# Kernel tuning notes

Hardware: AMD Instinct MI355X
Metric: run time of the kernel (lower is better)

The kernel has to match this reference:

```python
import jax, jax.numpy as jnp
import numpy as np

NEG_SLOPE = 0.2  # PyG GATConv default negative_slope
NUM_GRAPHS = 64
N, E, F_IN = 50000, 800000, 128


def _gat(x, src, dst, W, a_s, a_d, b, concat):
    # PyG GATConv: h = x W (per head); e_ij = leaky_relu(a_s.h_j + a_d.h_i);
    # softmax over incoming edges of each dst node; out_i = sum_j alpha_ij h_j
    n = x.shape[0]
    H, C = a_s.shape
    h = (x @ W).reshape(n, H, C)                     # [N,H,C]
    es = jnp.einsum('nhc,hc->nh', h, a_s)            # [N,H]
    ed = jnp.einsum('nhc,hc->nh', h, a_d)
    e = jax.nn.leaky_relu(es[src] + ed[dst], NEG_SLOPE)   # [E,H]
    m = jax.ops.segment_max(e, dst, num_segments=n)       # per-dst max (stable softmax)
    ex = jnp.exp(e - m[dst])
    den = jax.ops.segment_sum(ex, dst, num_segments=n)
    alpha = ex / den[dst]                                 # [E,H]
    out = jax.ops.segment_sum(h[src] * alpha[:, :, None], dst, num_segments=n)  # [N,H,C]
    if concat:
        return out.reshape(n, H * C) + b
    return out.mean(axis=1) + b


def setup_inputs() -> dict:
    key = jax.random.key(0)
    ks = jax.random.split(key, 10)
    x = jax.random.normal(ks[0], (N, F_IN), jnp.float32)
    edge_index = jax.random.randint(ks[1], (2, E), 0, N, dtype=jnp.int64)
    batch = jnp.sort(jax.random.randint(ks[2], (N,), 0, NUM_GRAPHS, dtype=jnp.int64))
    s1 = 1.0 / np.sqrt(F_IN)
    s2 = 1.0 / np.sqrt(256)
    return {
        'x': x,
        'edge_index': edge_index,
        'batch': batch,
        'W1': jax.random.normal(ks[3], (F_IN, 256), jnp.float32) * s1,
        'a_src1': jax.random.normal(ks[4], (4, 64), jnp.float32) * s2,
        'a_dst1': jax.random.normal(ks[5], (4, 64), jnp.float32) * s2,
        'b1': jnp.zeros((256,), jnp.float32),
        'W2': jax.random.normal(ks[6], (256, 128), jnp.float32) * s2,
        'a_src2': jax.random.normal(ks[7], (1, 128), jnp.float32) * (1.0 / np.sqrt(128)),
        'a_dst2': jax.random.normal(ks[8], (1, 128), jnp.float32) * (1.0 / np.sqrt(128)),
        'b2': jnp.zeros((128,), jnp.float32),
        'fc_w': jax.random.normal(ks[9], (128, 10), jnp.float32) * (1.0 / np.sqrt(128)),
        'fc_b': jnp.zeros((10,), jnp.float32),
    }


def reference(x, edge_index, batch, W1, a_src1, a_dst1, b1, W2, a_src2, a_dst2, b2, fc_w, fc_b):
    n = x.shape[0]
    loop = jnp.arange(n, dtype=edge_index.dtype)  # PyG add_self_loops=True
    src = jnp.concatenate([edge_index[0], loop])
    dst = jnp.concatenate([edge_index[1], loop])
    h = jax.nn.elu(_gat(x, src, dst, W1, a_src1, a_dst1, b1, True))   # dropout: eval mode -> identity
    h = jax.nn.elu(_gat(h, src, dst, W2, a_src2, a_dst2, b2, False))
    pooled = jax.ops.segment_sum(h, batch, num_segments=NUM_GRAPHS)
    cnt = jax.ops.segment_sum(jnp.ones((n,), h.dtype), batch, num_segments=NUM_GRAPHS)
    pooled = pooled / jnp.maximum(cnt, 1.0)[:, None]
    logits = pooled @ fc_w + fc_b
    return jax.nn.log_softmax(logits, axis=1)
```

## Files before the change

kernel.cpp:

```cpp
#include <hip/hip_runtime.h>
#include <math.h>

#define N_NODES 50000
#define N_PAD   50048
#define N_EDGES 800000
#define E_TOT   (N_EDGES + N_NODES)
#define NG 64
#define CAP 48
#define NBKT 512
#define BNODES 98
#define RCAP 24
#define FILL_CHUNK 2048
#define GEMM1_BLOCKS 782
#define FILL_BLOCKS  391
#define PH1_TOTAL (GEMM1_BLOCKS + FILL_BLOCKS)
#define G2_NB 16

typedef short short8 __attribute__((ext_vector_type(8)));
typedef float floatx4 __attribute__((ext_vector_type(4)));
typedef float floatx2 __attribute__((ext_vector_type(2)));

__device__ inline short f2bf(float f) {
    union { float f; unsigned u; } v; v.f = f;
    unsigned r = v.u + 0x7fff + ((v.u >> 16) & 1);
    return (short)(r >> 16);
}

__device__ inline unsigned f2fp8(float f) {
    union { float f; unsigned u; } v; v.f = f;
    unsigned s = v.u & 0x80000000u;
    unsigned au = v.u & 0x7fffffffu;
    if (au > 0x43E00000u) au = 0x43E00000u;
    unsigned r = au + 0x7ffffu + ((au >> 20) & 1);
    int e8 = (int)(r >> 23) - 120;
    unsigned m3 = (r >> 20) & 7;
    unsigned code;
    if (e8 <= 0) code = 0;
    else if (e8 > 15) code = 0x7e;
    else code = ((unsigned)e8 << 3) | m3;
    return (s >> 24) | code;
}

__device__ inline float leaky_exp(float t) {
    t = t > 0.f ? t : 0.2f * t;
    return __expf(t);
}

__device__ inline unsigned rfl(unsigned v) {
    return (unsigned)__builtin_amdgcn_readfirstlane((int)v);
}


__global__ __launch_bounds__(256) void phase1_kernel(const float* __restrict__ x,
                                                     const float* __restrict__ W1,
                                                     const float* __restrict__ a_s,
                                                     const float* __restrict__ a_d,
                                                     const int* __restrict__ ei,
                                                     unsigned short* __restrict__ gcnt,
                                                     unsigned* __restrict__ gb2,
                                                     unsigned char* __restrict__ C8,
                                                     float* __restrict__ es,
                                                     float* __restrict__ ed,
                                                     const float* __restrict__ W2,
                                                     const float* __restrict__ as2,
                                                     const float* __restrict__ ad2,
                                                     float* __restrict__ ws2,
                                                     float* __restrict__ wd2,
                                                     float* __restrict__ pooled) {
    __shared__ short bs[64][136];
    __shared__ int hist[NBKT];
    int bid = blockIdx.x;
    int tid = threadIdx.x;

    if (bid == PH1_TOTAL) {
        int k = tid;
        float s = 0.f, d = 0.f;
        for (int c = 0; c < 128; c++) {
            float w = W2[k * 128 + c];
            s += w * as2[c];
            d += w * ad2[c];
        }
        ws2[k] = s;
        wd2[k] = d;
        for (int i = tid; i < NG * 128; i += 256) pooled[i] = 0.f;
        return;
    }

    int gb = -1, fb = -1;
    {
        int g3 = bid / 3, r3 = bid - g3 * 3;
        if (r3 == 2) fb = g3;
        else         gb = g3 * 2 + r3;
    }

    if (fb >= 0) {
        hist[tid] = 0; hist[tid + 256] = 0;
        __syncthreads();
        unsigned meta[8], pay[8];
        int e0 = fb * FILL_CHUNK;
#pragma unroll
        for (int j = 0; j < 8; j++) {
            int t = e0 + j * 256 + tid;
            if (t < N_EDGES) {
                int s = ei[t];
                int d = ei[N_EDGES + t];
                unsigned bkt = (unsigned)d / 98u;
                int dlow = d - (int)bkt * 98;
                int pos = atomicAdd(&hist[bkt], 1);
                meta[j] = (bkt << 16) | (unsigned)pos;
                pay[j] = ((unsigned)s << 9) | (unsigned)dlow;
            } else {
                meta[j] = 0xffffffffu;
            }
        }
        __syncthreads();
        {
            int c0h = hist[tid];        if (c0h > RCAP) c0h = RCAP;
            int c1h = hist[tid + 256];  if (c1h > RCAP) c1h = RCAP;
            gcnt[fb * NBKT + tid] = (unsigned short)c0h;
            gcnt[fb * NBKT + tid + 256] = (unsigned short)c1h;
        }
#pragma unroll
        for (int j = 0; j < 8; j++) {
            if (meta[j] != 0xffffffffu) {
                unsigned bkt = meta[j] >> 16;
                unsigned pos = meta[j] & 0xffffu;
                if (pos < RCAP)
                    gb2[((size_t)bkt * FILL_BLOCKS + fb) * RCAP + pos] = pay[j];
            }
        }
        return;
    }

    const int K = 128, N = 256;
    int tc = tid & 63;
    int tk0s = (tid >> 6) * 32;
    int wid = tid >> 6;
    int lane = tid & 63;
    int m0 = gb * 64 + wid * 16;
    int mr = lane & 15;
    int quad = lane >> 4;
    int kq = quad << 3;
    int arow = m0 + mr; if (arow > N_NODES - 1) arow = N_NODES - 1;
    const float* aptr = x + (size_t)arow * K + kq;
    short8 a[4];
#pragma unroll
    for (int kk = 0; kk < 4; kk++) {
        float4 f0 = *(const float4*)(aptr + kk * 32);
        float4 f1 = *(const float4*)(aptr + kk * 32 + 4);
        a[kk][0] = f2bf(f0.x); a[kk][1] = f2bf(f0.y); a[kk][2] = f2bf(f0.z); a[kk][3] = f2bf(f0.w);
        a[kk][4] = f2bf(f1.x); a[kk][5] = f2bf(f1.y); a[kk][6] = f2bf(f1.z); a[kk][7] = f2bf(f1.w);
    }
    int orow = m0 + (quad << 2);
    for (int head = 0; head < 4; head++) {
        int c0 = head * 64;
        if (head) __syncthreads();
        for (int k = tk0s; k < tk0s + 32; k++)
            bs[tc][k] = f2bf(W1[k * 256 + c0 + tc]);
        __syncthreads();
        floatx4 acc[4] = {{0.f,0.f,0.f,0.f},{0.f,0.f,0.f,0.f},{0.f,0.f,0.f,0.f},{0.f,0.f,0.f,0.f}};
#pragma unroll
        for (int kk = 0; kk < 4; kk++) {
#pragma unroll
            for (int t = 0; t < 4; t++) {
                short8 b = *(const short8*)&bs[t * 16 + mr][kq + kk * 32];
                acc[t] = __builtin_amdgcn_mfma_f32_16x16x32_bf16(a[kk], b, acc[t], 0, 0, 0);
            }
        }
        float asv[4], adv[4];
#pragma unroll
        for (int t = 0; t < 4; t++) {
            asv[t] = a_s[c0 + t * 16 + mr];
            adv[t] = a_d[c0 + t * 16 + mr];
        }
#pragma unroll
        for (int r = 0; r < 4; r++) {
            float ps = acc[0][r] * asv[0] + acc[1][r] * asv[1] + acc[2][r] * asv[2] + acc[3][r] * asv[3];
            float pd = acc[0][r] * adv[0] + acc[1][r] * adv[1] + acc[2][r] * adv[2] + acc[3][r] * adv[3];
#pragma unroll
            for (int off = 8; off >= 1; off >>= 1) {
                ps += __shfl_xor(ps, off);
                pd += __shfl_xor(pd, off);
            }
            if (mr == 0) {
                es[(orow + r) * 4 + head] = ps;
                ed[(orow + r) * 4 + head] = pd;
            }
        }
#pragma unroll
        for (int t = 0; t < 4; t++) {
            int ocol = c0 + t * 16 + mr;
#pragma unroll
            for (int r = 0; r < 4; r++) {
                C8[(size_t)(orow + r) * N + ocol] = (unsigned char)f2fp8(acc[t][r]);
            }
        }
    }
}


__global__ __launch_bounds__(512) void binfill_kernel(const unsigned* __restrict__ gb2,
                                                      const unsigned short* __restrict__ gcnt,
                                                      unsigned short* __restrict__ col,
                                                      int* __restrict__ degT) {
    __shared__ unsigned colL[BNODES * CAP / 2];
    __shared__ int cnt[BNODES];
    __shared__ unsigned short cl[FILL_BLOCKS + 1];
    int b = blockIdx.x, tid = threadIdx.x;
    int nbase = b * BNODES;

    for (int i = tid; i < BNODES * CAP / 8; i += 512) ((uint4*)colL)[i] = make_uint4(0, 0, 0, 0);
    if (tid < FILL_BLOCKS) cl[tid] = gcnt[tid * NBKT + b];
    if (tid < BNODES) cnt[tid] = (nbase + tid < N_NODES) ? 1 : 0;
    __syncthreads();

    if (tid < BNODES) {
        int nn = nbase + tid;
        if (nn < N_NODES) ((unsigned short*)colL)[tid * CAP] = (unsigned short)nn;
    }
    const uint4* src4 = (const uint4*)(gb2 + (size_t)b * FILL_BLOCKS * RCAP);
    for (int r = tid; r < FILL_BLOCKS * RCAP / 4; r += 512) {
        int blk = r / 6;
        int q = r - blk * 6;
        int c = cl[blk];
        if (q * 4 < c) {
            uint4 v = src4[r];
            unsigned vv[4] = {v.x, v.y, v.z, v.w};
#pragma unroll
            for (int j = 0; j < 4; j++) {
                if (q * 4 + j < c) {
                    unsigned p = vv[j];
                    int dlow = (int)(p & 511u);
                    int s = (int)(p >> 9);
                    int sp = atomicAdd(&cnt[dlow], 1);
                    if (sp < CAP) ((unsigned short*)colL)[dlow * CAP + sp] = (unsigned short)s;
                }
            }
        }
    }
    __syncthreads();

    uint4* cb = (uint4*)(col + (size_t)b * BNODES * CAP);
    for (int i = tid; i < BNODES * CAP / 8; i += 512) cb[i] = ((uint4*)colL)[i];
    if (tid < BNODES) {
        int nn = nbase + tid;
        if (nn < N_NODES) degT[nn] = cnt[tid];
    }
}


__global__ __launch_bounds__(256) void gather1_kernel(const unsigned char* __restrict__ h8,
                                                      const int* __restrict__ degT,
                                                      const unsigned short* __restrict__ col,
                                                      const float* __restrict__ es,
                                                      const float* __restrict__ ed,
                                                      const float* __restrict__ bias,
                                                      const float* __restrict__ ws2,
                                                      const float* __restrict__ wd2,
                                                      short* __restrict__ out,
                                                      float* __restrict__ es2,
                                                      float* __restrict__ ed2) {
    __shared__ float wlds[4][CAP * 4];
    int tid = threadIdx.x;
    int wid = tid >> 6;
    int n = __builtin_amdgcn_readfirstlane(blockIdx.x * 4 + wid);
    int l = tid & 63;
    int hh = l >> 4;
    int cnt = degT[n]; cnt = cnt < CAP ? cnt : CAP;
    int cnt8 = (cnt + 7) & ~7;

    const uint4* cp4 = (const uint4*)(col + n * CAP);
    uint4 cw0 = cp4[0], cw1 = cp4[1], cw2 = cp4[2], cw3 = cp4[3], cw4 = cp4[4], cw5 = cp4[5];

    unsigned hvA[8], hvB[8];

#define G1_ISSUE(cw, hv) { \
    unsigned d0 = rfl(cw.x), d1 = rfl(cw.y), d2 = rfl(cw.z), d3 = rfl(cw.w); \
    unsigned i0 = d0 & 0xffffu, i1 = d0 >> 16, i2 = d1 & 0xffffu, i3 = d1 >> 16; \
    unsigned i4 = d2 & 0xffffu, i5 = d2 >> 16, i6 = d3 & 0xffffu, i7 = d3 >> 16; \
    hv[0] = *(const unsigned*)&h8[(size_t)i0 * 256 + l * 4]; \
    hv[1] = *(const unsigned*)&h8[(size_t)i1 * 256 + l * 4]; \
    hv[2] = *(const unsigned*)&h8[(size_t)i2 * 256 + l * 4]; \
    hv[3] = *(const unsigned*)&h8[(size_t)i3 * 256 + l * 4]; \
    hv[4] = *(const unsigned*)&h8[(size_t)i4 * 256 + l * 4]; \
    hv[5] = *(const unsigned*)&h8[(size_t)i5 * 256 + l * 4]; \
    hv[6] = *(const unsigned*)&h8[(size_t)i6 * 256 + l * 4]; \
    hv[7] = *(const unsigned*)&h8[(size_t)i7 * 256 + l * 4]; }

#define G1_CONS(eb, hv) { \
    _Pragma("unroll") \
    for (int j = 0; j < 8; j++) { \
        float w = wlds[wid][((eb) + j) * 4 + hh]; \
        floatx2 lo = __builtin_amdgcn_cvt_pk_f32_fp8(hv[j], false); \
        floatx2 hi = __builtin_amdgcn_cvt_pk_f32_fp8(hv[j], true); \
        den += w; ax += w * lo[0]; ay += w * lo[1]; az += w * hi[0]; aw += w * hi[1]; } }

    G1_ISSUE(cw0, hvA);
    if (cnt8 > 8) G1_ISSUE(cw1, hvB);

    {
        float4 edv = *(const float4*)&ed[n * 4];
        if (l < CAP) {
            int s = col[n * CAP + l];
            float4 ev = *(const float4*)&es[s * 4];
            float4 wv4;
            if (l < cnt) {
                wv4.x = leaky_exp(ev.x + edv.x);
                wv4.y = leaky_exp(ev.y + edv.y);
                wv4.z = leaky_exp(ev.z + edv.z);
                wv4.w = leaky_exp(ev.w + edv.w);
            } else {
                wv4.x = wv4.y = wv4.z = wv4.w = 0.f;
            }
            *(float4*)&wlds[wid][l * 4] = wv4;
        }
    }

    float ax = 0.f, ay = 0.f, az = 0.f, aw = 0.f, den = 0.f;
    G1_CONS(0, hvA);
    if (cnt8 > 8) {
        if (cnt8 > 16) G1_ISSUE(cw2, hvA);
        G1_CONS(8, hvB);
        if (cnt8 > 16) {
            if (cnt8 > 24) G1_ISSUE(cw3, hvB);
            G1_CONS(16, hvA);
            if (cnt8 > 24) {
                if (cnt8 > 32) G1_ISSUE(cw4, hvA);
                G1_CONS(24, hvB);
                if (cnt8 > 32) {
                    if (cnt8 > 40) G1_ISSUE(cw5, hvB);
                    G1_CONS(32, hvA);
                    if (cnt8 > 40) G1_CONS(40, hvB);
                }
            }
        }
    }
#undef G1_ISSUE
#undef G1_CONS

    float inv = 1.0f / den;
    float4 bb = *(const float4*)&bias[l * 4];
    float o0 = ax * inv + bb.x;
    float o1 = ay * inv + bb.y;
    float o2 = az * inv + bb.z;
    float o3 = aw * inv + bb.w;
    o0 = o0 > 0.f ? o0 : __expf(o0) - 1.f;
    o1 = o1 > 0.f ? o1 : __expf(o1) - 1.f;
    o2 = o2 > 0.f ? o2 : __expf(o2) - 1.f;
    o3 = o3 > 0.f ? o3 : __expf(o3) - 1.f;
    short4 ob;
    ob.x = f2bf(o0); ob.y = f2bf(o1); ob.z = f2bf(o2); ob.w = f2bf(o3);
    *(short4*)&out[(size_t)n * 256 + l * 4] = ob;

    float4 s4 = *(const float4*)&ws2[l * 4];
    float4 d4 = *(const float4*)&wd2[l * 4];
    float ps = o0 * s4.x + o1 * s4.y + o2 * s4.z + o3 * s4.w;
    float pd = o0 * d4.x + o1 * d4.y + o2 * d4.z + o3 * d4.w;
#pragma unroll
    for (int off = 32; off >= 1; off >>= 1) {
        ps += __shfl_xor(ps, off);
        pd += __shfl_xor(pd, off);
    }
    if (l == 0) {
        es2[n] = ps;
        ed2[n] = pd;
    }
}


__global__ __launch_bounds__(256) void gemm2_kernel(const short* __restrict__ A,
                                                    const float* __restrict__ W2,
                                                    unsigned char* __restrict__ C8) {
    __shared__ short bs[64][264];
    const int K = 256, N = 128;
    int tid = threadIdx.x;
    int tc = tid & 63;
    int tk0s = (tid >> 6) * 64;
    int wid = tid >> 6;
    int lane = tid & 63;
    int m0 = blockIdx.x * 64 + wid * 16;
    int mr = lane & 15;
    int quad = lane >> 4;
    int kq = quad << 3;
    const short* arow = A + (size_t)(m0 + mr) * K + kq;
    short8 a[8];
#pragma unroll
    for (int kk = 0; kk < 8; kk++) a[kk] = *(const short8*)(arow + kk * 32);
    int orow = m0 + (quad << 2);
    for (int by = 0; by < 2; by++) {
        int c0 = by * 64;
        if (by) __syncthreads();
        for (int k = tk0s; k < tk0s + 64; k++)
            bs[tc][k] = f2bf(W2[k * 128 + c0 + tc]);
        __syncthreads();
        floatx4 acc[4] = {{0.f,0.f,0.f,0.f},{0.f,0.f,0.f,0.f},{0.f,0.f,0.f,0.f},{0.f,0.f,0.f,0.f}};
#pragma unroll
        for (int kk = 0; kk < 8; kk++) {
#pragma unroll
            for (int t = 0; t < 4; t++) {
                short8 b = *(const short8*)&bs[t * 16 + mr][kq + kk * 32];
                acc[t] = __builtin_amdgcn_mfma_f32_16x16x32_bf16(a[kk], b, acc[t], 0, 0, 0);
            }
        }
#pragma unroll
        for (int t = 0; t < 4; t++) {
            int ocol = c0 + t * 16 + mr;
#pragma unroll
            for (int r = 0; r < 4; r++) {
                C8[(size_t)(orow + r) * N + ocol] = (unsigned char)f2fp8(acc[t][r]);
            }
        }
    }
}


__global__ __launch_bounds__(256) void gather2_kernel(const unsigned char* __restrict__ h8,
                                                      const int* __restrict__ deg,
                                                      const unsigned short* __restrict__ col,
                                                      const float* __restrict__ es2,
                                                      const float* __restrict__ ed2,
                                                      const float* __restrict__ bias,
                                                      const int* __restrict__ batch,
                                                      float* __restrict__ pooled) {
    __shared__ float wlds[4][CAP];
    __shared__ float plds[8][128];
    __shared__ int pg[8];
    __shared__ int pcnt;
    int tid = threadIdx.x;
    int wid = tid >> 6;
    int l = tid & 63;
    if (tid == 0) pcnt = 0;
    __syncthreads();

    int c0 = l * 2;
    float2 bb = *(const float2*)&bias[c0];
    int nbase = blockIdx.x * G2_NB + wid * (G2_NB / 4);
    int curg = -1;
    float a0 = 0.f, a1 = 0.f;

    auto flush = [&]() {
        if (curg >= 0) {
            int idx = 0;
            if (l == 0) idx = atomicAdd(&pcnt, 1);
            idx = __shfl(idx, 0);
            if (idx < 8) {
                if (l == 0) pg[idx] = curg;
                plds[idx][c0] = a0;
                plds[idx][c0 + 1] = a1;
            } else {
                atomicAdd(&pooled[curg * 128 + c0], a0);
                atomicAdd(&pooled[curg * 128 + c0 + 1], a1);
            }
        }
    };

    unsigned hvA[8], hvB[8];

#define G2_ISSUE(cw, hv) { \
    unsigned d0 = rfl(cw.x), d1 = rfl(cw.y), d2 = rfl(cw.z), d3 = rfl(cw.w); \
    unsigned i0 = d0 & 0xffffu, i1 = d0 >> 16, i2 = d1 & 0xffffu, i3 = d1 >> 16; \
    unsigned i4 = d2 & 0xffffu, i5 = d2 >> 16, i6 = d3 & 0xffffu, i7 = d3 >> 16; \
    hv[0] = *(const unsigned short*)&h8[(size_t)i0 * 128 + l * 2]; \
    hv[1] = *(const unsigned short*)&h8[(size_t)i1 * 128 + l * 2]; \
    hv[2] = *(const unsigned short*)&h8[(size_t)i2 * 128 + l * 2]; \
    hv[3] = *(const unsigned short*)&h8[(size_t)i3 * 128 + l * 2]; \
    hv[4] = *(const unsigned short*)&h8[(size_t)i4 * 128 + l * 2]; \
    hv[5] = *(const unsigned short*)&h8[(size_t)i5 * 128 + l * 2]; \
    hv[6] = *(const unsigned short*)&h8[(size_t)i6 * 128 + l * 2]; \
    hv[7] = *(const unsigned short*)&h8[(size_t)i7 * 128 + l * 2]; }

#define G2_CONS(eb, hv) { \
    _Pragma("unroll") \
    for (int j = 0; j < 8; j++) { \
        float w = wlds[wid][(eb) + j]; \
        floatx2 lo = __builtin_amdgcn_cvt_pk_f32_fp8(hv[j], false); \
        den += w; ax += w * lo[0]; ay += w * lo[1]; } }

    for (int i = 0; i < G2_NB / 4; i++) {
        int n = nbase + i;
        if (n < N_NODES) {
            int bg = batch[n];
            if (bg != curg) {
                flush();
                curg = bg; a0 = 0.f; a1 = 0.f;
            }
            int cnt = deg[n]; cnt = cnt < CAP ? cnt : CAP;
            int cnt8 = (cnt + 7) & ~7;
            const uint4* cp4 = (const uint4*)(col + n * CAP);
            uint4 cw0 = cp4[0], cw1 = cp4[1], cw2 = cp4[2];
            uint4 cw3 = cp4[3], cw4 = cp4[4], cw5 = cp4[5];
            float ax = 0.f, ay = 0.f, den = 0.f;

            G2_ISSUE(cw0, hvA);
            if (cnt8 > 8) G2_ISSUE(cw1, hvB);

            {
                float edv = ed2[n];
                if (l < CAP) {
                    int s = col[n * CAP + l];
                    float w = (l < cnt) ? leaky_exp(es2[s] + edv) : 0.f;
                    wlds[wid][l] = w;
                }
            }

            G2_CONS(0, hvA);
            if (cnt8 > 8) {
                if (cnt8 > 16) G2_ISSUE(cw2, hvA);
                G2_CONS(8, hvB);
                if (cnt8 > 16) {
                    if (cnt8 > 24) G2_ISSUE(cw3, hvB);
                    G2_CONS(16, hvA);
                    if (cnt8 > 24) {
                        if (cnt8 > 32) G2_ISSUE(cw4, hvA);
                        G2_CONS(24, hvB);
                        if (cnt8 > 32) {
                            if (cnt8 > 40) G2_ISSUE(cw5, hvB);
                            G2_CONS(32, hvA);
                            if (cnt8 > 40) G2_CONS(40, hvB);
                        }
                    }
                }
            }

            float inv = 1.0f / den;
            float o0 = ax * inv + bb.x;
            float o1 = ay * inv + bb.y;
            o0 = o0 > 0.f ? o0 : __expf(o0) - 1.f;
            o1 = o1 > 0.f ? o1 : __expf(o1) - 1.f;
            a0 += o0; a1 += o1;
        }
    }
#undef G2_ISSUE
#undef G2_CONS
    flush();
    __syncthreads();

    int m = pcnt; if (m > 8) m = 8;
    if (tid < 128) {
        for (int e = 0; e < m; e++) {
            int ge = pg[e];
            bool first = true;
            for (int e2 = 0; e2 < e; e2++) if (pg[e2] == ge) first = false;
            if (first) {
                float s = plds[e][tid];
                for (int e3 = e + 1; e3 < m; e3++) if (pg[e3] == ge) s += plds[e3][tid];
                atomicAdd(&pooled[ge * 128 + tid], s);
            }
        }
    }
}


__global__ void fc_kernel(const float* __restrict__ pooled, const int* __restrict__ batch,
                          const float* __restrict__ fcw, const float* __restrict__ fcb,
                          float* __restrict__ out) {
    int g = threadIdx.x;
    if (g >= NG) return;
    int lo = 0, hi = N_NODES;
    while (lo < hi) {
        int mid = (lo + hi) >> 1;
        if (batch[mid] < g) lo = mid + 1; else hi = mid;
    }
    int start = lo;
    lo = start; hi = N_NODES;
    while (lo < hi) {
        int mid = (lo + hi) >> 1;
        if (batch[mid] <= g) lo = mid + 1; else hi = mid;
    }
    int cnt = lo - start;
    float inv = 1.0f / (float)(cnt > 0 ? cnt : 1);

    float lg[10];
#pragma unroll
    for (int j = 0; j < 10; j++) lg[j] = fcb[j];
    for (int k = 0; k < 128; k++) {
        float p = pooled[g * 128 + k] * inv;
#pragma unroll
        for (int j = 0; j < 10; j++) lg[j] += p * fcw[k * 10 + j];
    }
    float m = lg[0];
#pragma unroll
    for (int j = 1; j < 10; j++) m = fmaxf(m, lg[j]);
    float se = 0.f;
#pragma unroll
    for (int j = 0; j < 10; j++) se += __expf(lg[j] - m);
    float lse = m + __logf(se);
#pragma unroll
    for (int j = 0; j < 10; j++) out[g * 10 + j] = lg[j] - lse;
}


extern "C" void kernel_launch(void* const* d_in, const int* in_sizes, int n_in,
                              void* d_out, int out_size, void* d_ws, size_t ws_size,
                              hipStream_t stream) {
    const float* x     = (const float*)d_in[0];
    const int*   ei    = (const int*)d_in[1];
    const int*   batch = (const int*)d_in[2];
    const float* W1    = (const float*)d_in[3];
    const float* as1   = (const float*)d_in[4];
    const float* ad1   = (const float*)d_in[5];
    const float* b1    = (const float*)d_in[6];
    const float* W2    = (const float*)d_in[7];
    const float* as2   = (const float*)d_in[8];
    const float* ad2   = (const float*)d_in[9];
    const float* b2    = (const float*)d_in[10];
    const float* fcw   = (const float*)d_in[11];
    const float* fcb   = (const float*)d_in[12];
    float* out = (float*)d_out;

    char* ws = (char*)d_ws;
    size_t off = 0;
    auto alloc = [&](size_t bytes) -> void* {
        void* p = ws + off;
        off = (off + bytes + 255) & ~(size_t)255;
        return p;
    };
    float* pooled        = (float*)alloc(NG * 128 * 4);
    int* degT            = (int*)alloc((size_t)N_PAD * 4);
    unsigned short* col  = (unsigned short*)alloc((size_t)NBKT * BNODES * CAP * 2);
    unsigned* gb2        = (unsigned*)alloc((size_t)NBKT * FILL_BLOCKS * RCAP * 4);
    unsigned short* gcnt = (unsigned short*)alloc((size_t)FILL_BLOCKS * NBKT * 2);
    float* es1           = (float*)alloc((size_t)N_PAD * 4 * 4);
    float* ed1           = (float*)alloc((size_t)N_PAD * 4 * 4);
    float* es2           = (float*)alloc((size_t)N_PAD * 4);
    float* ed2           = (float*)alloc((size_t)N_PAD * 4);
    float* ws2           = (float*)alloc(256 * 4);
    float* wd2           = (float*)alloc(256 * 4);
    unsigned char* h1    = (unsigned char*)alloc((size_t)N_PAD * 256);
    short* h1p           = (short*)alloc((size_t)N_PAD * 256 * 2);
    unsigned char* h2    = (unsigned char*)alloc((size_t)N_PAD * 128);

    phase1_kernel<<<PH1_TOTAL + 1, 256, 0, stream>>>(x, W1, as1, ad1, ei, gcnt, gb2, h1, es1, ed1,
                                                     W2, as2, ad2, ws2, wd2, pooled);
    binfill_kernel<<<NBKT, 512, 0, stream>>>(gb2, gcnt, col, degT);
    gather1_kernel<<<N_NODES / 4, 256, 0, stream>>>(h1, degT, col, es1, ed1, b1, ws2, wd2,
                                                    h1p, es2, ed2);
    gemm2_kernel<<<N_PAD / 64, 256, 0, stream>>>(h1p, W2, h2);
    gather2_kernel<<<(N_NODES + G2_NB - 1) / G2_NB, 256, 0, stream>>>(h2, degT, col, es2, ed2, b2,
                                                                      batch, pooled);
    fc_kernel<<<1, 64, 0, stream>>>(pooled, batch, fcw, fcb, out);
}
```

Baseline: 229.8 us.

## Fuse FC head into gather2 via last-block counter and interleave two nodes per wave

Removes the separate fc_kernel launch: gather2 blocks atomically increment a done counter, and the last block computes the pooled mean, FC and log-softmax. The gather loop now processes two nodes at once, issuing fp8 row loads for both before consuming them to raise memory-level parallelism. The node-bound check is dropped, relying on N_NODES being divisible by G2_NB. The counter is reset in phase1, and the last-block pattern adds a threadfence and an atomic to every block.

```diff
diff --git a/kernel.cpp b/kernel.cpp
--- a/kernel.cpp
+++ b/kernel.cpp
@@ -66,7 +66,8 @@
                                                      const float* __restrict__ ad2,
                                                      float* __restrict__ ws2,
                                                      float* __restrict__ wd2,
-                                                     float* __restrict__ pooled) {
+                                                     float* __restrict__ pooled,
+                                                     unsigned* __restrict__ done) {
     __shared__ short bs[64][136];
     __shared__ int hist[NBKT];
     int bid = blockIdx.x;
@@ -83,6 +84,7 @@
         ws2[k] = s;
         wd2[k] = d;
         for (int i = tid; i < NG * 128; i += 256) pooled[i] = 0.f;
+        if (tid == 0) done[0] = 0u;
         return;
     }
 
@@ -421,11 +423,16 @@
                                                       const float* __restrict__ ed2,
                                                       const float* __restrict__ bias,
                                                       const int* __restrict__ batch,
-                                                      float* __restrict__ pooled) {
-    __shared__ float wlds[4][CAP];
+                                                      float* __restrict__ pooled,
+                                                      const float* __restrict__ fcw,
+                                                      const float* __restrict__ fcb,
+                                                      float* __restrict__ outF,
+                                                      unsigned* __restrict__ done) {
+    __shared__ float wlds[4][2][CAP];
     __shared__ float plds[8][128];
     __shared__ int pg[8];
     __shared__ int pcnt;
+    __shared__ unsigned rankS;
     int tid = threadIdx.x;
     int wid = tid >> 6;
     int l = tid & 63;
@@ -434,7 +441,7 @@
 
     int c0 = l * 2;
     float2 bb = *(const float2*)&bias[c0];
-    int nbase = blockIdx.x * G2_NB + wid * (G2_NB / 4);
+    int nbase = blockIdx.x * G2_NB + wid * 4;
     int curg = -1;
     float a0 = 0.f, a1 = 0.f;
 
@@ -454,7 +461,7 @@
         }
     };
 
-    unsigned hvA[8], hvB[8];
+    unsigned hvA[8], hvB[8], hvC[8], hvD[8];
 
 #define G2_ISSUE(cw, hv) { \
     unsigned d0 = rfl(cw.x), d1 = rfl(cw.y), d2 = rfl(cw.z), d3 = rfl(cw.w); \
@@ -469,69 +476,88 @@
     hv[6] = *(const unsigned short*)&h8[(size_t)i6 * 128 + l * 2]; \
     hv[7] = *(const unsigned short*)&h8[(size_t)i7 * 128 + l * 2]; }
 
-#define G2_CONS(eb, hv) { \
+#define G2_CONS(eb, hv, nn) { \
     _Pragma("unroll") \
     for (int j = 0; j < 8; j++) { \
-        float w = wlds[wid][(eb) + j]; \
+        float w = wlds[wid][nn][(eb) + j]; \
         floatx2 lo = __builtin_amdgcn_cvt_pk_f32_fp8(hv[j], false); \
         den += w; ax += w * lo[0]; ay += w * lo[1]; } }
 
-    for (int i = 0; i < G2_NB / 4; i++) {
-        int n = nbase + i;
-        if (n < N_NODES) {
-            int bg = batch[n];
-            if (bg != curg) {
-                flush();
-                curg = bg; a0 = 0.f; a1 = 0.f;
-            }
-            int cnt = deg[n]; cnt = cnt < CAP ? cnt : CAP;
-            int cnt8 = (cnt + 7) & ~7;
-            const uint4* cp4 = (const uint4*)(col + n * CAP);
-            uint4 cw0 = cp4[0], cw1 = cp4[1], cw2 = cp4[2];
-            uint4 cw3 = cp4[3], cw4 = cp4[4], cw5 = cp4[5];
+#define G2_CHAIN(c8, cp, hvX, hvY, nn) { \
+    G2_CONS(0, hvX, nn); \
+    if ((c8) > 8) { \
+        if ((c8) > 16) { uint4 w = (cp)[2]; G2_ISSUE(w, hvX); } \
+        G2_CONS(8, hvY, nn); \
+        if ((c8) > 16) { \
+            if ((c8) > 24) { uint4 w = (cp)[3]; G2_ISSUE(w, hvY); } \
+            G2_CONS(16, hvX, nn); \
+            if ((c8) > 24) { \
+                if ((c8) > 32) { uint4 w = (cp)[4]; G2_ISSUE(w, hvX); } \
+                G2_CONS(24, hvY, nn); \
+                if ((c8) > 32) { \
+                    if ((c8) > 40) { uint4 w = (cp)[5]; G2_ISSUE(w, hvY); } \
+                    G2_CONS(32, hvX, nn); \
+                    if ((c8) > 40) G2_CONS(40, hvY, nn); \
+                } \
+            } \
+        } \
+    } }
+
+    for (int p = 0; p < 2; p++) {
+        int n0 = nbase + p * 2;
+        int n1 = n0 + 1;
+        int cnt0 = deg[n0]; cnt0 = cnt0 < CAP ? cnt0 : CAP;
+        int cnt1 = deg[n1]; cnt1 = cnt1 < CAP ? cnt1 : CAP;
+        int c8a = (cnt0 + 7) & ~7;
+        int c8b = (cnt1 + 7) & ~7;
+        const uint4* cpA = (const uint4*)(col + n0 * CAP);
+        const uint4* cpB = (const uint4*)(col + n1 * CAP);
+        uint4 wa0 = cpA[0], wa1 = cpA[1];
+        uint4 wb0 = cpB[0], wb1 = cpB[1];
+
+        G2_ISSUE(wa0, hvA);
+        if (c8a > 8) G2_ISSUE(wa1, hvB);
+        G2_ISSUE(wb0, hvC);
+        if (c8b > 8) G2_ISSUE(wb1, hvD);
+
+        {
+            float edv0 = ed2[n0], edv1 = ed2[n1];
+            if (l < CAP) {
+                int s0 = col[n0 * CAP + l];
+                int s1 = col[n1 * CAP + l];
+                wlds[wid][0][l] = (l < cnt0) ? leaky_exp(es2[s0] + edv0) : 0.f;
+                wlds[wid][1][l] = (l < cnt1) ? leaky_exp(es2[s1] + edv1) : 0.f;
+            }
+        }
+
+        {
             float ax = 0.f, ay = 0.f, den = 0.f;
-
-            G2_ISSUE(cw0, hvA);
-            if (cnt8 > 8) G2_ISSUE(cw1, hvB);
-
-            {
-                float edv = ed2[n];
-                if (l < CAP) {
-                    int s = col[n * CAP + l];
-                    float w = (l < cnt) ? leaky_exp(es2[s] + edv) : 0.f;
-                    wlds[wid][l] = w;
-                }
-            }
-
-            G2_CONS(0, hvA);
-            if (cnt8 > 8) {
-                if (cnt8 > 16) G2_ISSUE(cw2, hvA);
-                G2_CONS(8, hvB);
-                if (cnt8 > 16) {
-                    if (cnt8 > 24) G2_ISSUE(cw3, hvB);
-                    G2_CONS(16, hvA);
-                    if (cnt8 > 24) {
-                        if (cnt8 > 32) G2_ISSUE(cw4, hvA);
-                        G2_CONS(24, hvB);
-                        if (cnt8 > 32) {
-                            if (cnt8 > 40) G2_ISSUE(cw5, hvB);
-                            G2_CONS(32, hvA);
-                            if (cnt8 > 40) G2_CONS(40, hvB);
-                        }
-                    }
-                }
-            }
-
+            G2_CHAIN(c8a, cpA, hvA, hvB, 0);
             float inv = 1.0f / den;
             float o0 = ax * inv + bb.x;
             float o1 = ay * inv + bb.y;
             o0 = o0 > 0.f ? o0 : __expf(o0) - 1.f;
             o1 = o1 > 0.f ? o1 : __expf(o1) - 1.f;
+            int bg = batch[n0];
+            if (bg != curg) { flush(); curg = bg; a0 = 0.f; a1 = 0.f; }
+            a0 += o0; a1 += o1;
+        }
+        {
+            float ax = 0.f, ay = 0.f, den = 0.f;
+            G2_CHAIN(c8b, cpB, hvC, hvD, 1);
+            float inv = 1.0f / den;
+            float o0 = ax * inv + bb.x;
+            float o1 = ay * inv + bb.y;
+            o0 = o0 > 0.f ? o0 : __expf(o0) - 1.f;
+            o1 = o1 > 0.f ? o1 : __expf(o1) - 1.f;
+            int bg = batch[n1];
+            if (bg != curg) { flush(); curg = bg; a0 = 0.f; a1 = 0.f; }
             a0 += o0; a1 += o1;
         }
     }
 #undef G2_ISSUE
 #undef G2_CONS
+#undef G2_CHAIN
     flush();
     __syncthreads();
 
@@ -548,45 +574,46 @@
             }
         }
     }
-}
-
-
-__global__ void fc_kernel(const float* __restrict__ pooled, const int* __restrict__ batch,
-                          const float* __restrict__ fcw, const float* __restrict__ fcb,
-                          float* __restrict__ out) {
-    int g = threadIdx.x;
-    if (g >= NG) return;
-    int lo = 0, hi = N_NODES;
-    while (lo < hi) {
-        int mid = (lo + hi) >> 1;
-        if (batch[mid] < g) lo = mid + 1; else hi = mid;
-    }
-    int start = lo;
-    lo = start; hi = N_NODES;
-    while (lo < hi) {
-        int mid = (lo + hi) >> 1;
-        if (batch[mid] <= g) lo = mid + 1; else hi = mid;
-    }
-    int cnt = lo - start;
-    float inv = 1.0f / (float)(cnt > 0 ? cnt : 1);
-
-    float lg[10];
-#pragma unroll
-    for (int j = 0; j < 10; j++) lg[j] = fcb[j];
-    for (int k = 0; k < 128; k++) {
-        float p = pooled[g * 128 + k] * inv;
-#pragma unroll
-        for (int j = 0; j < 10; j++) lg[j] += p * fcw[k * 10 + j];
-    }
-    float m = lg[0];
-#pragma unroll
-    for (int j = 1; j < 10; j++) m = fmaxf(m, lg[j]);
-    float se = 0.f;
-#pragma unroll
-    for (int j = 0; j < 10; j++) se += __expf(lg[j] - m);
-    float lse = m + __logf(se);
-#pragma unroll
-    for (int j = 0; j < 10; j++) out[g * 10 + j] = lg[j] - lse;
+
+    __threadfence();
+    if (tid == 0) rankS = atomicAdd(done, 1u);
+    __syncthreads();
+    if (rankS == (unsigned)(gridDim.x - 1) && tid < NG) {
+        int g = tid;
+        int lo = 0, hi = N_NODES;
+        while (lo < hi) {
+            int mid = (lo + hi) >> 1;
+            if (batch[mid] < g) lo = mid + 1; else hi = mid;
+        }
+        int start = lo;
+        lo = start; hi = N_NODES;
+        while (lo < hi) {
+            int mid = (lo + hi) >> 1;
+            if (batch[mid] <= g) lo = mid + 1; else hi = mid;
+        }
+        int cnt = lo - start;
+        float inv = 1.0f / (float)(cnt > 0 ? cnt : 1);
+
+        float lg[10];
+#pragma unroll
+        for (int j = 0; j < 10; j++) lg[j] = fcb[j];
+        for (int k = 0; k < 128; k++) {
+            float pv = __hip_atomic_load(&pooled[g * 128 + k], __ATOMIC_RELAXED,
+                                         __HIP_MEMORY_SCOPE_AGENT);
+            float pp = pv * inv;
+#pragma unroll
+            for (int j = 0; j < 10; j++) lg[j] += pp * fcw[k * 10 + j];
+        }
+        float mx = lg[0];
+#pragma unroll
+        for (int j = 1; j < 10; j++) mx = fmaxf(mx, lg[j]);
+        float se = 0.f;
+#pragma unroll
+        for (int j = 0; j < 10; j++) se += __expf(lg[j] - mx);
+        float lse = mx + __logf(se);
+#pragma unroll
+        for (int j = 0; j < 10; j++) outF[g * 10 + j] = lg[j] - lse;
+    }
 }
 
 
@@ -616,6 +643,7 @@
         return p;
     };
     float* pooled        = (float*)alloc(NG * 128 * 4);
+    unsigned* done       = (unsigned*)alloc(256);
     int* degT            = (int*)alloc((size_t)N_PAD * 4);
     unsigned short* col  = (unsigned short*)alloc((size_t)NBKT * BNODES * CAP * 2);
     unsigned* gb2        = (unsigned*)alloc((size_t)NBKT * FILL_BLOCKS * RCAP * 4);
@@ -631,12 +659,11 @@
     unsigned char* h2    = (unsigned char*)alloc((size_t)N_PAD * 128);
 
     phase1_kernel<<<PH1_TOTAL + 1, 256, 0, stream>>>(x, W1, as1, ad1, ei, gcnt, gb2, h1, es1, ed1,
-                                                     W2, as2, ad2, ws2, wd2, pooled);
+                                                     W2, as2, ad2, ws2, wd2, pooled, done);
     binfill_kernel<<<NBKT, 512, 0, stream>>>(gb2, gcnt, col, degT);
     gather1_kernel<<<N_NODES / 4, 256, 0, stream>>>(h1, degT, col, es1, ed1, b1, ws2, wd2,
                                                     h1p, es2, ed2);
     gemm2_kernel<<<N_PAD / 64, 256, 0, stream>>>(h1p, W2, h2);
-    gather2_kernel<<<(N_NODES + G2_NB - 1) / G2_NB, 256, 0, stream>>>(h2, degT, col, es2, ed2, b2,
-                                                                      batch, pooled);
-    fc_kernel<<<1, 64, 0, stream>>>(pooled, batch, fcw, fcb, out);
-}
+    gather2_kernel<<<N_NODES / G2_NB, 256, 0, stream>>>(h2, degT, col, es2, ed2, b2,
+                                                        batch, pooled, fcw, fcb, out, done);
+}
```

New measurement: 463.6 us. 2.02x slower.
